# Kernel tuning notes

Measured on AMD Instinct MI355X. Metric: run time of the kernel, lower is better.

The kernel has to match this reference:

```python
import jax, jax.numpy as jnp
import numpy as np

C = 256
HEADS = 8
HD = C // HEADS
EPS = 1e-5


def _layernorm(x, g, b):
    mu = jnp.mean(x, axis=-1, keepdims=True)
    var = jnp.var(x, axis=-1, keepdims=True)
    return (x - mu) * jax.lax.rsqrt(var + EPS) * g + b


def setup_inputs() -> dict:
    key = jax.random.key(0)
    ks = jax.random.split(key, 16)
    s = 0.02
    return {
        "x": jax.random.normal(ks[0], (1, C, 64, 64), jnp.float32),
        "bn_gamma": 1.0 + s * jax.random.normal(ks[1], (C,), jnp.float32),
        "bn_beta": s * jax.random.normal(ks[2], (C,), jnp.float32),
        "bn_mean": s * jax.random.normal(ks[3], (C,), jnp.float32),
        "bn_var": jnp.ones((C,), jnp.float32),
        "w_in": s * jax.random.normal(ks[4], (C, C), jnp.float32),
        "b_in": jnp.zeros((C,), jnp.float32),
        "ln1_g": jnp.ones((C,), jnp.float32),
        "ln1_b": jnp.zeros((C,), jnp.float32),
        "w_qkv": s * jax.random.normal(ks[5], (3 * C, C), jnp.float32),
        "b_qkv": jnp.zeros((3 * C,), jnp.float32),
        "w_ap": s * jax.random.normal(ks[6], (C, C), jnp.float32),
        "b_ap": jnp.zeros((C,), jnp.float32),
        "ln2_g": jnp.ones((C,), jnp.float32),
        "ln2_b": jnp.zeros((C,), jnp.float32),
        "w_ff1": s * jax.random.normal(ks[7], (4 * C, C), jnp.float32),
        "b_ff1": jnp.zeros((4 * C,), jnp.float32),
        "w_ff2": s * jax.random.normal(ks[8], (C, 4 * C), jnp.float32),
        "b_ff2": jnp.zeros((C,), jnp.float32),
        "w_out": s * jax.random.normal(ks[9], (C, C), jnp.float32),
        "b_out": jnp.zeros((C,), jnp.float32),
    }


def reference(x, bn_gamma, bn_beta, bn_mean, bn_var, w_in, b_in,
              ln1_g, ln1_b, w_qkv, b_qkv, w_ap, b_ap,
              ln2_g, ln2_b, w_ff1, b_ff1, w_ff2, b_ff2, w_out, b_out):
    b, c, h, w = x.shape
    t = h * w
    x_in = x
    # BatchNorm2d (eval mode: running stats)
    xn = (x - bn_mean[None, :, None, None]) * jax.lax.rsqrt(bn_var + EPS)[None, :, None, None]
    xn = xn * bn_gamma[None, :, None, None] + bn_beta[None, :, None, None]
    # proj_in 1x1 conv -> tokens [b, t, c]
    tok = xn.reshape(b, c, t).transpose(0, 2, 1)
    tok = tok @ w_in.T + b_in
    # transformer block (depth=1)
    y = _layernorm(tok, ln1_g, ln1_b)  # norm1
    qkv = y @ w_qkv.T + b_qkv  # [b, t, 3c], channel split (3, H, hd)
    qkv = qkv.reshape(b, t, 3, HEADS, HD)
    q = qkv[:, :, 0].transpose(0, 2, 1, 3)  # [b, H, t, hd]
    k = qkv[:, :, 1].transpose(0, 2, 1, 3)
    v = qkv[:, :, 2].transpose(0, 2, 1, 3)
    scale = HD ** (-0.5)
    attn = jax.nn.softmax(jnp.einsum('bhqd,bhkd->bhqk', q, k) * scale, axis=-1)
    o = jnp.einsum('bhqk,bhkd->bhqd', attn, v)  # [b, H, t, hd]
    o = o.transpose(0, 2, 1, 3).reshape(b, t, c)  # channels ordered (H, hd)
    o = o @ w_ap.T + b_ap  # attn proj 1x1
    attn_out = o + y  # VanillaAttention residual adds its (normed) input
    tok = tok + attn_out
    # FFN
    z = _layernorm(tok, ln2_g, ln2_b)
    z = jax.nn.gelu(z @ w_ff1.T + b_ff1, approximate=False)
    tok = tok + (z @ w_ff2.T + b_ff2)
    # back to image, proj_out 1x1, outer residual
    x4 = tok.transpose(0, 2, 1).reshape(b, c, h, w)
    out = jnp.einsum('oc,bchw->bohw', w_out, x4) + b_out[None, :, None, None]
    return out + x_in
```

## Files before the change

kernel.cpp:

```cpp
#include <hip/hip_runtime.h>
#include <math.h>

#define T_TOK 4096
#define C_DIM 256
#define EPSF  1e-5f
#define SC_QL (0.17677669529663687f * 1.4426950408889634f)

typedef short  bf16x8  __attribute__((ext_vector_type(8)));
typedef float  f32x4   __attribute__((ext_vector_type(4)));
typedef ushort ushort8 __attribute__((ext_vector_type(8)));

__device__ __forceinline__ short f2bf(float f) {
    unsigned u = __builtin_bit_cast(unsigned, f);
    unsigned r = (u + 0x7FFFu + ((u >> 16) & 1u)) >> 16;
    return (short)r;
}
__device__ __forceinline__ float bf2f(ushort u) {
    return __builtin_bit_cast(float, ((unsigned)u) << 16);
}
__device__ __forceinline__ unsigned pk_bf16(float a, float b) {
    const unsigned ua = __builtin_bit_cast(unsigned, a) + 0x8000u;
    const unsigned ub = __builtin_bit_cast(unsigned, b) + 0x8000u;
    return __builtin_amdgcn_perm(ub, ua, 0x07060302u);
}
#define MFMA16(a, b, c) __builtin_amdgcn_mfma_f32_16x16x32_bf16(a, b, c, 0, 0, 0)

__global__ __launch_bounds__(256) void prep_kernel(
    const float* __restrict__ w_in, const float* __restrict__ w_qkv,
    const float* __restrict__ w_ap, const float* __restrict__ w_ff1,
    const float* __restrict__ w_ff2, const float* __restrict__ w_out,
    const float* __restrict__ b_qkv, const float* __restrict__ b_ff1,
    const float* __restrict__ ln1_g, const float* __restrict__ ln1_b,
    const float* __restrict__ ln2_g, const float* __restrict__ ln2_b,
    ushort* __restrict__ wbuf, float* __restrict__ u_all, float* __restrict__ d_all,
    const float* __restrict__ x, const float* __restrict__ gamma,
    const float* __restrict__ beta, const float* __restrict__ mean,
    const float* __restrict__ var, ushort* __restrict__ tin)
{
    __shared__ float tile[32][33];
    if (blockIdx.x < 896) {
        const int gid = blockIdx.x * 256 + threadIdx.x;
        const int e0 = gid * 4;
        const float* src; int off;
        float4 sc = {1.f, 1.f, 1.f, 1.f};
        if (e0 < 65536)       { src = w_in;  off = e0; }
        else if (e0 < 262144) {
            src = w_qkv; off = e0 - 65536;
            sc = *(const float4*)(ln1_g + (off & 255));
            if (off < 65536) { sc.x *= SC_QL; sc.y *= SC_QL; sc.z *= SC_QL; sc.w *= SC_QL; }
        }
        else if (e0 < 327680) { src = w_ap;  off = e0 - 262144; }
        else if (e0 < 589824) {
            src = w_ff1; off = e0 - 327680;
            sc = *(const float4*)(ln2_g + (off & 255));
        }
        else if (e0 < 851968) { src = w_ff2; off = e0 - 589824; }
        else                  { src = w_out; off = e0 - 851968; }
        const float4 v = *(const float4*)(src + off);
        ushort4 o;
        o.x = (ushort)f2bf(v.x * sc.x); o.y = (ushort)f2bf(v.y * sc.y);
        o.z = (ushort)f2bf(v.z * sc.z); o.w = (ushort)f2bf(v.w * sc.w);
        *(ushort4*)(wbuf + e0) = o;
    } else if (blockIdx.x < 1920) {
        const int bidx = blockIdx.x - 896;
        const int t0 = (bidx & 127) * 32, c0 = (bidx >> 7) * 32;
        const int tx = threadIdx.x & 31, ty = threadIdx.x >> 5;
#pragma unroll
        for (int i = 0; i < 32; i += 8) {
            const int c = c0 + ty + i;
            const float a = rsqrtf(var[c] + EPSF) * gamma[c];
            const float d = beta[c] - mean[c] * a;
            tile[ty + i][tx] = x[c * T_TOK + t0 + tx] * a + d;
        }
        __syncthreads();
#pragma unroll
        for (int i = 0; i < 32; i += 8) {
            const int t = t0 + ty + i;
            tin[t * C_DIM + c0 + tx] = (ushort)f2bf(tile[tx][ty + i]);
        }
    } else {
        const int row = (blockIdx.x - 1920) * 4 + (threadIdx.x >> 6);
        const int lane = threadIdx.x & 63;
        const float* W; const float* gv; const float* bv; float bias; float qs = 1.f;
        if (row < 768) {
            W = w_qkv + (size_t)row * 256; gv = ln1_g; bv = ln1_b; bias = b_qkv[row];
            if (row < 256) qs = SC_QL;
        } else {
            const int r2 = row - 768;
            W = w_ff1 + (size_t)r2 * 256; gv = ln2_g; bv = ln2_b; bias = b_ff1[r2];
        }
        const float4 w4 = *(const float4*)(W + lane * 4);
        const float4 g4 = *(const float4*)(gv + lane * 4);
        const float4 b4 = *(const float4*)(bv + lane * 4);
        float su = w4.x * g4.x + w4.y * g4.y + w4.z * g4.z + w4.w * g4.w;
        float sd = w4.x * b4.x + w4.y * b4.y + w4.z * b4.z + w4.w * b4.w;
#pragma unroll
        for (int off = 32; off > 0; off >>= 1) {
            su += __shfl_xor(su, off);
            sd += __shfl_xor(sd, off);
        }
        if (lane == 0) {
            u_all[row] = qs * su;
            d_all[row] = qs * (sd + bias);
        }
    }
}

__global__ __launch_bounds__(256) void k_lnstats(
    const float* __restrict__ in, float* __restrict__ st)
{
    const int row = blockIdx.x * 4 + (threadIdx.x >> 6);
    const int lane = threadIdx.x & 63;
    const float4 v = *(const float4*)(in + (size_t)row * 256 + lane * 4);
    float s  = v.x + v.y + v.z + v.w;
    float s2 = v.x * v.x + v.y * v.y + v.z * v.z + v.w * v.w;
#pragma unroll
    for (int off = 32; off > 0; off >>= 1) {
        s  += __shfl_xor(s, off);
        s2 += __shfl_xor(s2, off);
    }
    if (lane == 0) {
        const float mu = s * (1.0f / 256.0f);
        const float var = s2 * (1.0f / 256.0f) - mu * mu;
        st[(size_t)row * 2 + 0] = mu;
        st[(size_t)row * 2 + 1] = rsqrtf(var + EPSF);
    }
}


__global__ __launch_bounds__(256) void k_proj_in(
    const ushort* __restrict__ tin, const ushort* __restrict__ wb,
    const float* __restrict__ bias, float* __restrict__ tok0,
    ushort* __restrict__ vbuf)
{
    __shared__ ushort Wlds[64 * 264];
    __shared__ ushort At[2][16 * 264];
    const int chunk = blockIdx.x & 3, strip = blockIdx.x >> 2;
    const int tid = threadIdx.x, wv = tid >> 6, lane = tid & 63;
    const int c = lane & 15, g = lane >> 4;

    {
        const int wr = tid >> 2, wc = (tid & 3) * 64;
        const ushort* wp = wb + (size_t)(chunk * 64 + wr) * 256 + wc;
#pragma unroll
        for (int i = 0; i < 8; ++i)
            *(ushort8*)&Wlds[wr * 264 + wc + i * 8] = *(const ushort8*)(wp + i * 8);
    }
    const int r = tid >> 4, c0a = (tid & 15) * 16;
    const int t0 = strip * 64;
    ushort8 pre0 = *(const ushort8*)(tin + (size_t)(t0 + r) * 256 + c0a);
    ushort8 pre1 = *(const ushort8*)(tin + (size_t)(t0 + r) * 256 + c0a + 8);

    const int col = chunk * 64 + wv * 16 + c;
    const float bb = bias[col];
    int p = 0;
#pragma unroll
    for (int tile = 0; tile < 4; ++tile) {
        *(ushort8*)&At[p][r * 264 + c0a] = pre0;
        *(ushort8*)&At[p][r * 264 + c0a + 8] = pre1;
        __syncthreads();
        if (tile < 3) {
            pre0 = *(const ushort8*)(tin + (size_t)(t0 + 16 * (tile + 1) + r) * 256 + c0a);
            pre1 = *(const ushort8*)(tin + (size_t)(t0 + 16 * (tile + 1) + r) * 256 + c0a + 8);
        }
        f32x4 acc = {};
#pragma unroll
        for (int kc = 0; kc < 8; ++kc) {
            const bf16x8 af = *(const bf16x8*)&At[p][c * 264 + kc * 32 + g * 8];
            const bf16x8 wf = *(const bf16x8*)&Wlds[(wv * 16 + c) * 264 + kc * 32 + g * 8];
            acc = MFMA16(af, wf, acc);
        }
        const int tt = t0 + tile * 16;
#pragma unroll
        for (int rr = 0; rr < 4; ++rr) {
            const float v = acc[rr] + bb;
            const size_t idx = (size_t)(tt + 4 * g + rr) * 256 + col;
            tok0[idx] = v;
            vbuf[idx] = (ushort)f2bf(v);
        }
        p ^= 1;
    }
}

__global__ __launch_bounds__(256) void k_qkv(
    const ushort* __restrict__ vbuf, const ushort* __restrict__ wb,
    const float* __restrict__ lnst, const float* __restrict__ u_all,
    const float* __restrict__ d_all, ushort* __restrict__ qkvb)
{
    __shared__ ushort Wlds[64 * 264];
    __shared__ ushort At[2][16 * 264];
    const int chunk = blockIdx.x % 12, strip = blockIdx.x / 12;
    const int tid = threadIdx.x, wv = tid >> 6, lane = tid & 63;
    const int c = lane & 15, g = lane >> 4;

    {
        const int wr = tid >> 2, wc = (tid & 3) * 64;
        const ushort* wp = wb + (size_t)(chunk * 64 + wr) * 256 + wc;
#pragma unroll
        for (int i = 0; i < 8; ++i)
            *(ushort8*)&Wlds[wr * 264 + wc + i * 8] = *(const ushort8*)(wp + i * 8);
    }
    const int r = tid >> 4, c0a = (tid & 15) * 16;
    const int t0 = strip * 128;
    ushort8 pre0 = *(const ushort8*)(vbuf + (size_t)(t0 + r) * 256 + c0a);
    ushort8 pre1 = *(const ushort8*)(vbuf + (size_t)(t0 + r) * 256 + c0a + 8);

    const int col = chunk * 64 + wv * 16 + c;
    const float u = u_all[col], d = d_all[col];
    int p = 0;
#pragma unroll 1
    for (int tile = 0; tile < 8; ++tile) {
        *(ushort8*)&At[p][r * 264 + c0a] = pre0;
        *(ushort8*)&At[p][r * 264 + c0a + 8] = pre1;
        __syncthreads();
        if (tile < 7) {
            pre0 = *(const ushort8*)(vbuf + (size_t)(t0 + 16 * (tile + 1) + r) * 256 + c0a);
            pre1 = *(const ushort8*)(vbuf + (size_t)(t0 + 16 * (tile + 1) + r) * 256 + c0a + 8);
        }
        f32x4 acc = {};
#pragma unroll
        for (int kc = 0; kc < 8; ++kc) {
            const bf16x8 af = *(const bf16x8*)&At[p][c * 264 + kc * 32 + g * 8];
            const bf16x8 wf = *(const bf16x8*)&Wlds[(wv * 16 + c) * 264 + kc * 32 + g * 8];
            acc = MFMA16(af, wf, acc);
        }
        const int tt = t0 + tile * 16;
#pragma unroll
        for (int rr = 0; rr < 4; ++rr) {
            const int row = tt + 4 * g + rr;
            const float mu = lnst[(size_t)row * 2 + 0];
            const float rs = lnst[(size_t)row * 2 + 1];
            qkvb[(size_t)row * 768 + col] = (ushort)f2bf(rs * (acc[rr] - mu * u) + d);
        }
        p ^= 1;
    }
}

__global__ __launch_bounds__(256) void k_attnproj(
    const ushort* __restrict__ opart, const float* __restrict__ lpart,
    const ushort* __restrict__ wb, const float* __restrict__ bias,
    const float* __restrict__ tok0, const float* __restrict__ lnst,
    const float* __restrict__ ln1_g, const float* __restrict__ ln1_b,
    float* __restrict__ tok1, ushort* __restrict__ v2buf)
{
    __shared__ ushort Wlds[64 * 264];
    __shared__ ushort At[2][16 * 264];
    const int chunk = blockIdx.x & 3, strip = blockIdx.x >> 2;
    const int tid = threadIdx.x, wv = tid >> 6, lane = tid & 63;
    const int c = lane & 15, g = lane >> 4;

    {
        const int wr = tid >> 2, wc = (tid & 3) * 64;
        const ushort* wp = wb + (size_t)(chunk * 64 + wr) * 256 + wc;
#pragma unroll
        for (int i = 0; i < 8; ++i)
            *(ushort8*)&Wlds[wr * 264 + wc + i * 8] = *(const ushort8*)(wp + i * 8);
    }
    const int r = tid >> 4, c0a = (tid & 15) * 16;
    const int hh = c0a >> 5;
    const int t0 = strip * 64;

    ushort4 pa[4][4];
    float linv;
    {
        const float* lp = lpart + (size_t)(t0 + r) * 32;
        linv = 1.0f / (lp[hh] + lp[8 + hh] + lp[16 + hh] + lp[24 + hh]);
        const size_t base = (size_t)(t0 + r) * 256 + c0a;
#pragma unroll
        for (int cc = 0; cc < 4; ++cc)
#pragma unroll
            for (int q = 0; q < 4; ++q)
                pa[cc][q] = *(const ushort4*)(opart + ((size_t)q << 20) + base + cc * 4);
    }

    const int col = chunk * 64 + wv * 16 + c;
    const float bb = bias[col];
    const float g1 = ln1_g[col], b1 = ln1_b[col];
    int p = 0;
#pragma unroll
    for (int tile = 0; tile < 4; ++tile) {
#pragma unroll
        for (int cc = 0; cc < 4; ++cc) {
            unsigned w[2];
            w[0] = pk_bf16((bf2f(pa[cc][0].x) + bf2f(pa[cc][1].x) + bf2f(pa[cc][2].x) + bf2f(pa[cc][3].x)) * linv,
                           (bf2f(pa[cc][0].y) + bf2f(pa[cc][1].y) + bf2f(pa[cc][2].y) + bf2f(pa[cc][3].y)) * linv);
            w[1] = pk_bf16((bf2f(pa[cc][0].z) + bf2f(pa[cc][1].z) + bf2f(pa[cc][2].z) + bf2f(pa[cc][3].z)) * linv,
                           (bf2f(pa[cc][0].w) + bf2f(pa[cc][1].w) + bf2f(pa[cc][2].w) + bf2f(pa[cc][3].w)) * linv);
            *(ushort4*)&At[p][r * 264 + c0a + cc * 4] = *(ushort4*)w;
        }
        __syncthreads();
        if (tile < 3) {
            const int tn = t0 + 16 * (tile + 1);
            const float* lp = lpart + (size_t)(tn + r) * 32;
            linv = 1.0f / (lp[hh] + lp[8 + hh] + lp[16 + hh] + lp[24 + hh]);
            const size_t base = (size_t)(tn + r) * 256 + c0a;
#pragma unroll
            for (int cc = 0; cc < 4; ++cc)
#pragma unroll
                for (int q = 0; q < 4; ++q)
                    pa[cc][q] = *(const ushort4*)(opart + ((size_t)q << 20) + base + cc * 4);
        }
        f32x4 acc = {};
#pragma unroll
        for (int kc = 0; kc < 8; ++kc) {
            const bf16x8 af = *(const bf16x8*)&At[p][c * 264 + kc * 32 + g * 8];
            const bf16x8 wf = *(const bf16x8*)&Wlds[(wv * 16 + c) * 264 + kc * 32 + g * 8];
            acc = MFMA16(af, wf, acc);
        }
        const int tt = t0 + tile * 16;
#pragma unroll
        for (int rr = 0; rr < 4; ++rr) {
            const int row = tt + 4 * g + rr;
            const size_t idx = (size_t)row * 256 + col;
            const float t0v = tok0[idx];
            const float mu = lnst[(size_t)row * 2 + 0];
            const float rs = lnst[(size_t)row * 2 + 1];
            const float y = (t0v - mu) * rs * g1 + b1;
            const float v = acc[rr] + bb + y + t0v;
            tok1[idx] = v;
            v2buf[idx] = (ushort)f2bf(v);
        }
        p ^= 1;
    }
}

__global__ __launch_bounds__(256) void k_ff1(
    const ushort* __restrict__ v2buf, const ushort* __restrict__ wb,
    const float* __restrict__ lnst, const float* __restrict__ u_all,
    const float* __restrict__ d_all, ushort* __restrict__ zbuf)
{
    __shared__ ushort Wlds[64 * 264];
    __shared__ ushort At[2][16 * 264];
    const int chunk = blockIdx.x & 15, strip = blockIdx.x >> 4;
    const int tid = threadIdx.x, wv = tid >> 6, lane = tid & 63;
    const int c = lane & 15, g = lane >> 4;

    {
        const int wr = tid >> 2, wc = (tid & 3) * 64;
        const ushort* wp = wb + (size_t)(chunk * 64 + wr) * 256 + wc;
#pragma unroll
        for (int i = 0; i < 8; ++i)
            *(ushort8*)&Wlds[wr * 264 + wc + i * 8] = *(const ushort8*)(wp + i * 8);
    }
    const int r = tid >> 4, c0a = (tid & 15) * 16;
    const int t0 = strip * 128;
    ushort8 pre0 = *(const ushort8*)(v2buf + (size_t)(t0 + r) * 256 + c0a);
    ushort8 pre1 = *(const ushort8*)(v2buf + (size_t)(t0 + r) * 256 + c0a + 8);

    const int col = chunk * 64 + wv * 16 + c;
    const float u = u_all[768 + col], d = d_all[768 + col];
    int p = 0;
#pragma unroll 1
    for (int tile = 0; tile < 8; ++tile) {
        *(ushort8*)&At[p][r * 264 + c0a] = pre0;
        *(ushort8*)&At[p][r * 264 + c0a + 8] = pre1;
        __syncthreads();
        if (tile < 7) {
            pre0 = *(const ushort8*)(v2buf + (size_t)(t0 + 16 * (tile + 1) + r) * 256 + c0a);
            pre1 = *(const ushort8*)(v2buf + (size_t)(t0 + 16 * (tile + 1) + r) * 256 + c0a + 8);
        }
        f32x4 acc = {};
#pragma unroll
        for (int kc = 0; kc < 8; ++kc) {
            const bf16x8 af = *(const bf16x8*)&At[p][c * 264 + kc * 32 + g * 8];
            const bf16x8 wf = *(const bf16x8*)&Wlds[(wv * 16 + c) * 264 + kc * 32 + g * 8];
            acc = MFMA16(af, wf, acc);
        }
        const int tt = t0 + tile * 16;
#pragma unroll
        for (int rr = 0; rr < 4; ++rr) {
            const int row = tt + 4 * g + rr;
            const float mu = lnst[(size_t)row * 2 + 0];
            const float rs = lnst[(size_t)row * 2 + 1];
            float v = rs * (acc[rr] - mu * u) + d;
            v = 0.5f * v * (1.0f + erff(v * 0.70710678118654752f));
            zbuf[(size_t)row * 1024 + col] = (ushort)f2bf(v);
        }
        p ^= 1;
    }
}

__global__ __launch_bounds__(256) void k_ff2(
    const ushort* __restrict__ zbuf, const ushort* __restrict__ wb,
    const float* __restrict__ bias, const float* __restrict__ tok1,
    ushort* __restrict__ tok2)
{
    __shared__ ushort Wlds[32 * 1032];
    __shared__ ushort At[32 * 1032];
    const int chunk = blockIdx.x & 7, strip = blockIdx.x >> 3;
    const int tid = threadIdx.x, wv = tid >> 6, lane = tid & 63;
    const int c = lane & 15, g = lane >> 4;

    {
        const int wr = tid >> 3, wc = (tid & 7) * 128;
        const ushort* wp = wb + (size_t)(chunk * 32 + wr) * 1024 + wc;
#pragma unroll
        for (int i = 0; i < 16; ++i)
            *(ushort8*)&Wlds[wr * 1032 + wc + i * 8] = *(const ushort8*)(wp + i * 8);
    }
    const int r = tid >> 3, c0a = (tid & 7) * 128;
    const int t0 = strip * 128;
    ushort8 preZ[16];
#pragma unroll
    for (int i = 0; i < 16; ++i)
        preZ[i] = *(const ushort8*)(zbuf + (size_t)(t0 + r) * 1024 + c0a + i * 8);

    const int sub = wv >> 1, cw = (wv & 1) * 16;
    const int col = chunk * 32 + cw + c;
    const float bb = bias[col];
#pragma unroll 1
    for (int it = 0; it < 4; ++it) {
#pragma unroll
        for (int i = 0; i < 16; ++i)
            *(ushort8*)&At[r * 1032 + c0a + i * 8] = preZ[i];
        __syncthreads();
        if (it < 3) {
            const int tn = t0 + 32 * (it + 1);
#pragma unroll
            for (int i = 0; i < 16; ++i)
                preZ[i] = *(const ushort8*)(zbuf + (size_t)(tn + r) * 1024 + c0a + i * 8);
        }
        f32x4 acc = {};
#pragma unroll
        for (int kc = 0; kc < 32; ++kc) {
            const bf16x8 af = *(const bf16x8*)&At[(sub * 16 + c) * 1032 + kc * 32 + g * 8];
            const bf16x8 wf = *(const bf16x8*)&Wlds[(cw + c) * 1032 + kc * 32 + g * 8];
            acc = MFMA16(af, wf, acc);
        }
        const int tt = t0 + it * 32 + sub * 16;
#pragma unroll
        for (int rr = 0; rr < 4; ++rr) {
            const size_t idx = (size_t)(tt + 4 * g + rr) * 256 + col;
            tok2[idx] = (ushort)f2bf(acc[rr] + bb + tok1[idx]);
        }
        __syncthreads();
    }
}

__global__ __launch_bounds__(256) void k_pout(
    const ushort* __restrict__ tok2, const ushort* __restrict__ wb,
    const float* __restrict__ b_out, const float* __restrict__ x,
    float* __restrict__ out)
{
    __shared__ ushort Wlds[64 * 264];
    __shared__ ushort At[2][16 * 264];
    const int chunk = blockIdx.x & 3, strip = blockIdx.x >> 2;
    const int tid = threadIdx.x, wv = tid >> 6, lane = tid & 63;
    const int c = lane & 15, g = lane >> 4;

    {
        const int wr = tid >> 2, wc = (tid & 3) * 64;
        const ushort* wp = wb + (size_t)(chunk * 64 + wr) * 256 + wc;
#pragma unroll
        for (int i = 0; i < 8; ++i)
            *(ushort8*)&Wlds[wr * 264 + wc + i * 8] = *(const ushort8*)(wp + i * 8);
    }
    const int r = tid >> 4, c0a = (tid & 15) * 16;
    const int t0 = strip * 64;
    ushort8 pre0 = *(const ushort8*)(tok2 + (size_t)(t0 + r) * 256 + c0a);
    ushort8 pre1 = *(const ushort8*)(tok2 + (size_t)(t0 + r) * 256 + c0a + 8);

    int p = 0;
#pragma unroll
    for (int tile = 0; tile < 4; ++tile) {
        *(ushort8*)&At[p][r * 264 + c0a] = pre0;
        *(ushort8*)&At[p][r * 264 + c0a + 8] = pre1;
        __syncthreads();
        if (tile < 3) {
            pre0 = *(const ushort8*)(tok2 + (size_t)(t0 + 16 * (tile + 1) + r) * 256 + c0a);
            pre1 = *(const ushort8*)(tok2 + (size_t)(t0 + 16 * (tile + 1) + r) * 256 + c0a + 8);
        }
        f32x4 acc = {};
#pragma unroll
        for (int kc = 0; kc < 8; ++kc) {
            const bf16x8 wf = *(const bf16x8*)&Wlds[(wv * 16 + c) * 264 + kc * 32 + g * 8];
            const bf16x8 bf = *(const bf16x8*)&At[p][c * 264 + kc * 32 + g * 8];
            acc = MFMA16(wf, bf, acc);
        }
        const int tt = t0 + tile * 16;
#pragma unroll
        for (int rr = 0; rr < 4; ++rr) {
            const int och = chunk * 64 + wv * 16 + 4 * g + rr;
            const size_t idx = (size_t)och * T_TOK + tt + c;
            out[idx] = acc[rr] + b_out[och] + x[idx];
        }
        p ^= 1;
    }
}

#define KS   40
#define VTS  72
#define PS_W 34

__global__ __launch_bounds__(256) void attn_mfma(
    const ushort* __restrict__ qkv, ushort* __restrict__ opart,
    float* __restrict__ lpart)
{
    const int h    = blockIdx.y;
    const int q0   = blockIdx.x << 6;
    const int half = blockIdx.z;
    const int tid  = threadIdx.x;
    const int wv   = tid >> 6, lane = tid & 63;
    const int c    = lane & 15, g = lane >> 4;

    __shared__ ushort Ks[2][64 * KS];
    __shared__ ushort Vt[2][32 * VTS];
    __shared__ float  Ps[4][16 * PS_W];

    const bf16x8 qf = *(const bf16x8*)(qkv + (size_t)(q0 + wv * 16 + c) * 768 + h * 32 + g * 8);

    bf16x8 ones;
#pragma unroll
    for (int i = 0; i < 8; ++i) ones[i] = (short)0x3F80;

    f32x4 oacc0 = {0.f, 0.f, 0.f, 0.f};
    f32x4 oacc1 = {0.f, 0.f, 0.f, 0.f};
    f32x4 oaccl = {0.f, 0.f, 0.f, 0.f};

    const int kr = tid >> 2, kc = (tid & 3) * 8;
    const int vp = tid & 31, vd = (tid >> 5) * 4;
    const ushort* kbase = qkv + 256 + h * 32;
    const ushort* vbase = qkv + 512 + h * 32;

    const int kt0 = half * 16, kt1 = kt0 + 16;
    ushort8 kpre  = *(const ushort8*)(kbase + ((size_t)kt0 * 64 + kr) * 768 + kc);
    ushort4 vpre0 = *(const ushort4*)(vbase + ((size_t)kt0 * 64 + 2 * vp) * 768 + vd);
    ushort4 vpre1 = *(const ushort4*)(vbase + ((size_t)kt0 * 64 + 2 * vp + 1) * 768 + vd);

    int p = 0;
    for (int kt = kt0; kt < kt1; ++kt) {
        *(ushort8*)&Ks[p][kr * KS + kc] = kpre;
        {
            unsigned* vtp = (unsigned*)&Vt[p][0];
            vtp[(vd + 0) * (VTS / 2) + vp] = (unsigned)vpre0.x | ((unsigned)vpre1.x << 16);
            vtp[(vd + 1) * (VTS / 2) + vp] = (unsigned)vpre0.y | ((unsigned)vpre1.y << 16);
            vtp[(vd + 2) * (VTS / 2) + vp] = (unsigned)vpre0.z | ((unsigned)vpre1.z << 16);
            vtp[(vd + 3) * (VTS / 2) + vp] = (unsigned)vpre0.w | ((unsigned)vpre1.w << 16);
        }
        __syncthreads();
        if (kt + 1 < kt1) {
            const size_t t0 = (size_t)(kt + 1) * 64;
            kpre  = *(const ushort8*)(kbase + (t0 + kr) * 768 + kc);
            vpre0 = *(const ushort4*)(vbase + (t0 + 2 * vp) * 768 + vd);
            vpre1 = *(const ushort4*)(vbase + (t0 + 2 * vp + 1) * 768 + vd);
        }

        const ushort* ks = &Ks[p][0];
        const ushort* vt = &Vt[p][0];
        const f32x4 zz = {0.f, 0.f, 0.f, 0.f};
        const bf16x8 k0 = *(const bf16x8*)&ks[(0 * 16 + c) * KS + g * 8];
        const bf16x8 k1 = *(const bf16x8*)&ks[(1 * 16 + c) * KS + g * 8];
        const bf16x8 k2 = *(const bf16x8*)&ks[(2 * 16 + c) * KS + g * 8];
        const bf16x8 k3 = *(const bf16x8*)&ks[(3 * 16 + c) * KS + g * 8];
        const f32x4 s0 = MFMA16(k0, qf, zz);
        const f32x4 s1 = MFMA16(k1, qf, zz);
        const f32x4 s2 = MFMA16(k2, qf, zz);
        const f32x4 s3 = MFMA16(k3, qf, zz);

        float* prow = &Ps[wv][c * PS_W];
        {
            const float e00 = __builtin_amdgcn_exp2f(s0[0]), e01 = __builtin_amdgcn_exp2f(s0[1]);
            const float e02 = __builtin_amdgcn_exp2f(s0[2]), e03 = __builtin_amdgcn_exp2f(s0[3]);
            const float e10 = __builtin_amdgcn_exp2f(s1[0]), e11 = __builtin_amdgcn_exp2f(s1[1]);
            const float e12 = __builtin_amdgcn_exp2f(s1[2]), e13 = __builtin_amdgcn_exp2f(s1[3]);
            const float e20 = __builtin_amdgcn_exp2f(s2[0]), e21 = __builtin_amdgcn_exp2f(s2[1]);
            const float e22 = __builtin_amdgcn_exp2f(s2[2]), e23 = __builtin_amdgcn_exp2f(s2[3]);
            const float e30 = __builtin_amdgcn_exp2f(s3[0]), e31 = __builtin_amdgcn_exp2f(s3[1]);
            const float e32 = __builtin_amdgcn_exp2f(s3[2]), e33 = __builtin_amdgcn_exp2f(s3[3]);
            prow[0 * 8 + 2 * g + 0] = __builtin_bit_cast(float, pk_bf16(e00, e01));
            prow[0 * 8 + 2 * g + 1] = __builtin_bit_cast(float, pk_bf16(e02, e03));
            prow[1 * 8 + 2 * g + 0] = __builtin_bit_cast(float, pk_bf16(e10, e11));
            prow[1 * 8 + 2 * g + 1] = __builtin_bit_cast(float, pk_bf16(e12, e13));
            prow[2 * 8 + 2 * g + 0] = __builtin_bit_cast(float, pk_bf16(e20, e21));
            prow[2 * 8 + 2 * g + 1] = __builtin_bit_cast(float, pk_bf16(e22, e23));
            prow[3 * 8 + 2 * g + 0] = __builtin_bit_cast(float, pk_bf16(e30, e31));
            prow[3 * 8 + 2 * g + 1] = __builtin_bit_cast(float, pk_bf16(e32, e33));
        }
#pragma unroll
        for (int ch = 0; ch < 2; ++ch) {
            const float2 pA = *(const float2*)&prow[ch * 16 + 4 * g];
            const float2 pB = *(const float2*)&prow[ch * 16 + 4 * g + 2];
            unsigned pw[4];
            pw[0] = __builtin_bit_cast(unsigned, pA.x);
            pw[1] = __builtin_bit_cast(unsigned, pA.y);
            pw[2] = __builtin_bit_cast(unsigned, pB.x);
            pw[3] = __builtin_bit_cast(unsigned, pB.y);
            const bf16x8 pf = *(const bf16x8*)pw;
            const bf16x8 v0 = *(const bf16x8*)&vt[(c)      * VTS + ch * 32 + g * 8];
            const bf16x8 v1 = *(const bf16x8*)&vt[(16 + c) * VTS + ch * 32 + g * 8];
            oacc0 = MFMA16(pf, v0, oacc0);
            oacc1 = MFMA16(pf, v1, oacc1);
            oaccl = MFMA16(pf, ones, oaccl);
        }
        p ^= 1;
        __syncthreads();
    }

    {
        ushort* op = opart + (size_t)half * (1u << 20) + (size_t)(q0 + wv * 16) * 256 + h * 32;
#pragma unroll
        for (int rr = 0; rr < 4; ++rr) {
            op[(4 * g + rr) * 256 + c]      = (ushort)f2bf(oacc0[rr]);
            op[(4 * g + rr) * 256 + 16 + c] = (ushort)f2bf(oacc1[rr]);
        }
        if (c == 0) {
#pragma unroll
            for (int rr = 0; rr < 4; ++rr)
                lpart[(size_t)(q0 + wv * 16 + 4 * g + rr) * 32 + half * 8 + h] = oaccl[rr];
        }
    }
}

extern "C" void kernel_launch(void* const* d_in, const int* in_sizes, int n_in,
                              void* d_out, int out_size, void* d_ws, size_t ws_size,
                              hipStream_t stream)
{
    const float* x     = (const float*)d_in[0];
    const float* bn_g  = (const float*)d_in[1];
    const float* bn_b  = (const float*)d_in[2];
    const float* bn_m  = (const float*)d_in[3];
    const float* bn_v  = (const float*)d_in[4];
    const float* w_in  = (const float*)d_in[5];
    const float* b_in  = (const float*)d_in[6];
    const float* ln1_g = (const float*)d_in[7];
    const float* ln1_b = (const float*)d_in[8];
    const float* w_qkv = (const float*)d_in[9];
    const float* b_qkv = (const float*)d_in[10];
    const float* w_ap  = (const float*)d_in[11];
    const float* b_ap  = (const float*)d_in[12];
    const float* ln2_g = (const float*)d_in[13];
    const float* ln2_b = (const float*)d_in[14];
    const float* w_ff1 = (const float*)d_in[15];
    const float* b_ff1 = (const float*)d_in[16];
    const float* w_ff2 = (const float*)d_in[17];
    const float* b_ff2 = (const float*)d_in[18];
    const float* w_out = (const float*)d_in[19];
    const float* b_out = (const float*)d_in[20];
    float* out = (float*)d_out;
    float* ws  = (float*)d_ws;

    const size_t MF = 1u << 20;
    float*  tok0   = ws;
    float*  tok1   = ws + MF;
    float*  lnst1  = ws + 2 * MF;
    float*  lnst2  = ws + 2 * MF + 8192;
    ushort* tok2   = (ushort*)(ws + 2 * MF + MF / 4);
    ushort* vbuf   = (ushort*)(ws + 2 * MF + MF / 2);
    ushort* qkv_bf = (ushort*)(ws + 3 * MF);
    ushort* tin_bf = (ushort*)(ws + 4 * MF + MF / 2);
    ushort* opart  = tin_bf;
    ushort* v2buf  = (ushort*)(ws + 6 * MF + MF / 2);
    ushort* zbuf   = (ushort*)(ws + 7 * MF);
    float*  lpart  = ws + 9 * MF;
    ushort* wbuf   = (ushort*)(ws + 9 * MF + 131072);
    const ushort* wb_in  = wbuf;
    const ushort* wb_qkv = wbuf + 65536;
    const ushort* wb_ap  = wbuf + 262144;
    const ushort* wb_ff1 = wbuf + 327680;
    const ushort* wb_ff2 = wbuf + 589824;
    const ushort* wb_out = wbuf + 851968;
    float* u_all = (float*)(wbuf + 917504);
    float* d_all = u_all + 1792;

    prep_kernel<<<2368, 256, 0, stream>>>(
        w_in, w_qkv, w_ap, w_ff1, w_ff2, w_out,
        b_qkv, b_ff1, ln1_g, ln1_b, ln2_g, ln2_b,
        wbuf, u_all, d_all,
        x, bn_g, bn_b, bn_m, bn_v, tin_bf);
    k_proj_in<<<256, 256, 0, stream>>>(tin_bf, wb_in, b_in, tok0, vbuf);
    k_lnstats<<<1024, 256, 0, stream>>>(tok0, lnst1);
    k_qkv<<<384, 256, 0, stream>>>(vbuf, wb_qkv, lnst1, u_all, d_all, qkv_bf);
    attn_mfma<<<dim3(64, 8, 4), 256, 0, stream>>>(qkv_bf, opart, lpart);
    k_attnproj<<<256, 256, 0, stream>>>(opart, lpart, wb_ap, b_ap, tok0, lnst1,
                                        ln1_g, ln1_b, tok1, v2buf);
    k_lnstats<<<1024, 256, 0, stream>>>(tok1, lnst2);
    k_ff1<<<512, 256, 0, stream>>>(v2buf, wb_ff1, lnst2, u_all, d_all, zbuf);
    k_ff2<<<256, 256, 0, stream>>>(zbuf, wb_ff2, b_ff2, tok1, tok2);
    k_pout<<<256, 256, 0, stream>>>(tok2, wb_out, b_out, x, out);
}
```

Measured before the change: 215.1 us.

## Hold weights in registers, shrink token strips, split-K FF2 with fused residual in pout

```diff
diff --git a/kernel.cpp b/kernel.cpp
--- a/kernel.cpp
+++ b/kernel.cpp
@@ -133,52 +133,34 @@
     const float* __restrict__ bias, float* __restrict__ tok0,
     ushort* __restrict__ vbuf)
 {
-    __shared__ ushort Wlds[64 * 264];
-    __shared__ ushort At[2][16 * 264];
+    __shared__ ushort At[16 * 264];
     const int chunk = blockIdx.x & 3, strip = blockIdx.x >> 2;
     const int tid = threadIdx.x, wv = tid >> 6, lane = tid & 63;
     const int c = lane & 15, g = lane >> 4;
-
+    const int col = chunk * 64 + wv * 16 + c;
+    const int t0 = strip * 16;
+
+    bf16x8 w[8];
+#pragma unroll
+    for (int kc = 0; kc < 8; ++kc)
+        w[kc] = *(const bf16x8*)(wb + (size_t)col * 256 + kc * 32 + g * 8);
     {
-        const int wr = tid >> 2, wc = (tid & 3) * 64;
-        const ushort* wp = wb + (size_t)(chunk * 64 + wr) * 256 + wc;
-#pragma unroll
-        for (int i = 0; i < 8; ++i)
-            *(ushort8*)&Wlds[wr * 264 + wc + i * 8] = *(const ushort8*)(wp + i * 8);
-    }
-    const int r = tid >> 4, c0a = (tid & 15) * 16;
-    const int t0 = strip * 64;
-    ushort8 pre0 = *(const ushort8*)(tin + (size_t)(t0 + r) * 256 + c0a);
-    ushort8 pre1 = *(const ushort8*)(tin + (size_t)(t0 + r) * 256 + c0a + 8);
-
-    const int col = chunk * 64 + wv * 16 + c;
+        const int r = tid >> 4, c0 = (tid & 15) * 16;
+        *(ushort8*)&At[r * 264 + c0]     = *(const ushort8*)(tin + (size_t)(t0 + r) * 256 + c0);
+        *(ushort8*)&At[r * 264 + c0 + 8] = *(const ushort8*)(tin + (size_t)(t0 + r) * 256 + c0 + 8);
+    }
+    __syncthreads();
+    f32x4 acc = {};
+#pragma unroll
+    for (int kc = 0; kc < 8; ++kc)
+        acc = MFMA16(*(const bf16x8*)&At[c * 264 + kc * 32 + g * 8], w[kc], acc);
     const float bb = bias[col];
-    int p = 0;
-#pragma unroll
-    for (int tile = 0; tile < 4; ++tile) {
-        *(ushort8*)&At[p][r * 264 + c0a] = pre0;
-        *(ushort8*)&At[p][r * 264 + c0a + 8] = pre1;
-        __syncthreads();
-        if (tile < 3) {
-            pre0 = *(const ushort8*)(tin + (size_t)(t0 + 16 * (tile + 1) + r) * 256 + c0a);
-            pre1 = *(const ushort8*)(tin + (size_t)(t0 + 16 * (tile + 1) + r) * 256 + c0a + 8);
-        }
-        f32x4 acc = {};
-#pragma unroll
-        for (int kc = 0; kc < 8; ++kc) {
-            const bf16x8 af = *(const bf16x8*)&At[p][c * 264 + kc * 32 + g * 8];
-            const bf16x8 wf = *(const bf16x8*)&Wlds[(wv * 16 + c) * 264 + kc * 32 + g * 8];
-            acc = MFMA16(af, wf, acc);
-        }
-        const int tt = t0 + tile * 16;
-#pragma unroll
-        for (int rr = 0; rr < 4; ++rr) {
-            const float v = acc[rr] + bb;
-            const size_t idx = (size_t)(tt + 4 * g + rr) * 256 + col;
-            tok0[idx] = v;
-            vbuf[idx] = (ushort)f2bf(v);
-        }
-        p ^= 1;
+#pragma unroll
+    for (int rr = 0; rr < 4; ++rr) {
+        const float v = acc[rr] + bb;
+        const size_t idx = (size_t)(t0 + 4 * g + rr) * 256 + col;
+        tok0[idx] = v;
+        vbuf[idx] = (ushort)f2bf(v);
     }
 }
 
@@ -187,43 +169,35 @@
     const float* __restrict__ lnst, const float* __restrict__ u_all,
     const float* __restrict__ d_all, ushort* __restrict__ qkvb)
 {
-    __shared__ ushort Wlds[64 * 264];
     __shared__ ushort At[2][16 * 264];
     const int chunk = blockIdx.x % 12, strip = blockIdx.x / 12;
     const int tid = threadIdx.x, wv = tid >> 6, lane = tid & 63;
     const int c = lane & 15, g = lane >> 4;
-
-    {
-        const int wr = tid >> 2, wc = (tid & 3) * 64;
-        const ushort* wp = wb + (size_t)(chunk * 64 + wr) * 256 + wc;
-#pragma unroll
-        for (int i = 0; i < 8; ++i)
-            *(ushort8*)&Wlds[wr * 264 + wc + i * 8] = *(const ushort8*)(wp + i * 8);
-    }
-    const int r = tid >> 4, c0a = (tid & 15) * 16;
-    const int t0 = strip * 128;
-    ushort8 pre0 = *(const ushort8*)(vbuf + (size_t)(t0 + r) * 256 + c0a);
-    ushort8 pre1 = *(const ushort8*)(vbuf + (size_t)(t0 + r) * 256 + c0a + 8);
-
     const int col = chunk * 64 + wv * 16 + c;
+    const int t0 = strip * 32;
+    const int r = tid >> 4, c0 = (tid & 15) * 16;
+
+    bf16x8 w[8];
+#pragma unroll
+    for (int kc = 0; kc < 8; ++kc)
+        w[kc] = *(const bf16x8*)(wb + (size_t)col * 256 + kc * 32 + g * 8);
+    ushort8 pre0 = *(const ushort8*)(vbuf + (size_t)(t0 + r) * 256 + c0);
+    ushort8 pre1 = *(const ushort8*)(vbuf + (size_t)(t0 + r) * 256 + c0 + 8);
+
     const float u = u_all[col], d = d_all[col];
-    int p = 0;
-#pragma unroll 1
-    for (int tile = 0; tile < 8; ++tile) {
-        *(ushort8*)&At[p][r * 264 + c0a] = pre0;
-        *(ushort8*)&At[p][r * 264 + c0a + 8] = pre1;
+#pragma unroll
+    for (int tile = 0; tile < 2; ++tile) {
+        *(ushort8*)&At[tile][r * 264 + c0]     = pre0;
+        *(ushort8*)&At[tile][r * 264 + c0 + 8] = pre1;
         __syncthreads();
-        if (tile < 7) {
-            pre0 = *(const ushort8*)(vbuf + (size_t)(t0 + 16 * (tile + 1) + r) * 256 + c0a);
-            pre1 = *(const ushort8*)(vbuf + (size_t)(t0 + 16 * (tile + 1) + r) * 256 + c0a + 8);
+        if (tile == 0) {
+            pre0 = *(const ushort8*)(vbuf + (size_t)(t0 + 16 + r) * 256 + c0);
+            pre1 = *(const ushort8*)(vbuf + (size_t)(t0 + 16 + r) * 256 + c0 + 8);
         }
         f32x4 acc = {};
 #pragma unroll
-        for (int kc = 0; kc < 8; ++kc) {
-            const bf16x8 af = *(const bf16x8*)&At[p][c * 264 + kc * 32 + g * 8];
-            const bf16x8 wf = *(const bf16x8*)&Wlds[(wv * 16 + c) * 264 + kc * 32 + g * 8];
-            acc = MFMA16(af, wf, acc);
-        }
+        for (int kc = 0; kc < 8; ++kc)
+            acc = MFMA16(*(const bf16x8*)&At[tile][c * 264 + kc * 32 + g * 8], w[kc], acc);
         const int tt = t0 + tile * 16;
 #pragma unroll
         for (int rr = 0; rr < 4; ++rr) {
@@ -232,7 +206,6 @@
             const float rs = lnst[(size_t)row * 2 + 1];
             qkvb[(size_t)row * 768 + col] = (ushort)f2bf(rs * (acc[rr] - mu * u) + d);
         }
-        p ^= 1;
     }
 }
 
@@ -243,84 +216,55 @@
     const float* __restrict__ ln1_g, const float* __restrict__ ln1_b,
     float* __restrict__ tok1, ushort* __restrict__ v2buf)
 {
-    __shared__ ushort Wlds[64 * 264];
-    __shared__ ushort At[2][16 * 264];
+    __shared__ ushort At[16 * 264];
     const int chunk = blockIdx.x & 3, strip = blockIdx.x >> 2;
     const int tid = threadIdx.x, wv = tid >> 6, lane = tid & 63;
     const int c = lane & 15, g = lane >> 4;
-
+    const int col = chunk * 64 + wv * 16 + c;
+    const int t0 = strip * 16;
+
+    bf16x8 w[8];
+#pragma unroll
+    for (int kc = 0; kc < 8; ++kc)
+        w[kc] = *(const bf16x8*)(wb + (size_t)col * 256 + kc * 32 + g * 8);
     {
-        const int wr = tid >> 2, wc = (tid & 3) * 64;
-        const ushort* wp = wb + (size_t)(chunk * 64 + wr) * 256 + wc;
-#pragma unroll
-        for (int i = 0; i < 8; ++i)
-            *(ushort8*)&Wlds[wr * 264 + wc + i * 8] = *(const ushort8*)(wp + i * 8);
-    }
-    const int r = tid >> 4, c0a = (tid & 15) * 16;
-    const int hh = c0a >> 5;
-    const int t0 = strip * 64;
-
-    ushort4 pa[4][4];
-    float linv;
-    {
+        const int r = tid >> 4, c0 = (tid & 15) * 16;
+        const int hh = c0 >> 5;
         const float* lp = lpart + (size_t)(t0 + r) * 32;
-        linv = 1.0f / (lp[hh] + lp[8 + hh] + lp[16 + hh] + lp[24 + hh]);
-        const size_t base = (size_t)(t0 + r) * 256 + c0a;
-#pragma unroll
-        for (int cc = 0; cc < 4; ++cc)
-#pragma unroll
-            for (int q = 0; q < 4; ++q)
-                pa[cc][q] = *(const ushort4*)(opart + ((size_t)q << 20) + base + cc * 4);
-    }
-
-    const int col = chunk * 64 + wv * 16 + c;
+        const float inv = 1.0f / (lp[hh] + lp[8 + hh] + lp[16 + hh] + lp[24 + hh]);
+        const size_t base = (size_t)(t0 + r) * 256 + c0;
+#pragma unroll
+        for (int cc = 0; cc < 4; ++cc) {
+            const ushort4 a0 = *(const ushort4*)(opart + base + cc * 4);
+            const ushort4 a1 = *(const ushort4*)(opart + (1u << 20) + base + cc * 4);
+            const ushort4 a2 = *(const ushort4*)(opart + (2u << 20) + base + cc * 4);
+            const ushort4 a3 = *(const ushort4*)(opart + (3u << 20) + base + cc * 4);
+            unsigned wpk[2];
+            wpk[0] = pk_bf16((bf2f(a0.x) + bf2f(a1.x) + bf2f(a2.x) + bf2f(a3.x)) * inv,
+                             (bf2f(a0.y) + bf2f(a1.y) + bf2f(a2.y) + bf2f(a3.y)) * inv);
+            wpk[1] = pk_bf16((bf2f(a0.z) + bf2f(a1.z) + bf2f(a2.z) + bf2f(a3.z)) * inv,
+                             (bf2f(a0.w) + bf2f(a1.w) + bf2f(a2.w) + bf2f(a3.w)) * inv);
+            *(ushort4*)&At[r * 264 + c0 + cc * 4] = *(ushort4*)wpk;
+        }
+    }
+    __syncthreads();
+    f32x4 acc = {};
+#pragma unroll
+    for (int kc = 0; kc < 8; ++kc)
+        acc = MFMA16(*(const bf16x8*)&At[c * 264 + kc * 32 + g * 8], w[kc], acc);
     const float bb = bias[col];
     const float g1 = ln1_g[col], b1 = ln1_b[col];
-    int p = 0;
-#pragma unroll
-    for (int tile = 0; tile < 4; ++tile) {
-#pragma unroll
-        for (int cc = 0; cc < 4; ++cc) {
-            unsigned w[2];
-            w[0] = pk_bf16((bf2f(pa[cc][0].x) + bf2f(pa[cc][1].x) + bf2f(pa[cc][2].x) + bf2f(pa[cc][3].x)) * linv,
-                           (bf2f(pa[cc][0].y) + bf2f(pa[cc][1].y) + bf2f(pa[cc][2].y) + bf2f(pa[cc][3].y)) * linv);
-            w[1] = pk_bf16((bf2f(pa[cc][0].z) + bf2f(pa[cc][1].z) + bf2f(pa[cc][2].z) + bf2f(pa[cc][3].z)) * linv,
-                           (bf2f(pa[cc][0].w) + bf2f(pa[cc][1].w) + bf2f(pa[cc][2].w) + bf2f(pa[cc][3].w)) * linv);
-            *(ushort4*)&At[p][r * 264 + c0a + cc * 4] = *(ushort4*)w;
-        }
-        __syncthreads();
-        if (tile < 3) {
-            const int tn = t0 + 16 * (tile + 1);
-            const float* lp = lpart + (size_t)(tn + r) * 32;
-            linv = 1.0f / (lp[hh] + lp[8 + hh] + lp[16 + hh] + lp[24 + hh]);
-            const size_t base = (size_t)(tn + r) * 256 + c0a;
-#pragma unroll
-            for (int cc = 0; cc < 4; ++cc)
-#pragma unroll
-                for (int q = 0; q < 4; ++q)
-                    pa[cc][q] = *(const ushort4*)(opart + ((size_t)q << 20) + base + cc * 4);
-        }
-        f32x4 acc = {};
-#pragma unroll
-        for (int kc = 0; kc < 8; ++kc) {
-            const bf16x8 af = *(const bf16x8*)&At[p][c * 264 + kc * 32 + g * 8];
-            const bf16x8 wf = *(const bf16x8*)&Wlds[(wv * 16 + c) * 264 + kc * 32 + g * 8];
-            acc = MFMA16(af, wf, acc);
-        }
-        const int tt = t0 + tile * 16;
-#pragma unroll
-        for (int rr = 0; rr < 4; ++rr) {
-            const int row = tt + 4 * g + rr;
-            const size_t idx = (size_t)row * 256 + col;
-            const float t0v = tok0[idx];
-            const float mu = lnst[(size_t)row * 2 + 0];
-            const float rs = lnst[(size_t)row * 2 + 1];
-            const float y = (t0v - mu) * rs * g1 + b1;
-            const float v = acc[rr] + bb + y + t0v;
-            tok1[idx] = v;
-            v2buf[idx] = (ushort)f2bf(v);
-        }
-        p ^= 1;
+#pragma unroll
+    for (int rr = 0; rr < 4; ++rr) {
+        const int row = t0 + 4 * g + rr;
+        const size_t idx = (size_t)row * 256 + col;
+        const float t0v = tok0[idx];
+        const float mu = lnst[(size_t)row * 2 + 0];
+        const float rs = lnst[(size_t)row * 2 + 1];
+        const float y = (t0v - mu) * rs * g1 + b1;
+        const float v = acc[rr] + bb + y + t0v;
+        tok1[idx] = v;
+        v2buf[idx] = (ushort)f2bf(v);
     }
 }
 
@@ -329,43 +273,35 @@
     const float* __restrict__ lnst, const float* __restrict__ u_all,
     const float* __restrict__ d_all, ushort* __restrict__ zbuf)
 {
-    __shared__ ushort Wlds[64 * 264];
     __shared__ ushort At[2][16 * 264];
     const int chunk = blockIdx.x & 15, strip = blockIdx.x >> 4;
     const int tid = threadIdx.x, wv = tid >> 6, lane = tid & 63;
     const int c = lane & 15, g = lane >> 4;
-
-    {
-        const int wr = tid >> 2, wc = (tid & 3) * 64;
-        const ushort* wp = wb + (size_t)(chunk * 64 + wr) * 256 + wc;
-#pragma unroll
-        for (int i = 0; i < 8; ++i)
-            *(ushort8*)&Wlds[wr * 264 + wc + i * 8] = *(const ushort8*)(wp + i * 8);
-    }
-    const int r = tid >> 4, c0a = (tid & 15) * 16;
-    const int t0 = strip * 128;
-    ushort8 pre0 = *(const ushort8*)(v2buf + (size_t)(t0 + r) * 256 + c0a);
-    ushort8 pre1 = *(const ushort8*)(v2buf + (size_t)(t0 + r) * 256 + c0a + 8);
-
     const int col = chunk * 64 + wv * 16 + c;
+    const int t0 = strip * 32;
+    const int r = tid >> 4, c0 = (tid & 15) * 16;
+
+    bf16x8 w[8];
+#pragma unroll
+    for (int kc = 0; kc < 8; ++kc)
+        w[kc] = *(const bf16x8*)(wb + (size_t)col * 256 + kc * 32 + g * 8);
+    ushort8 pre0 = *(const ushort8*)(v2buf + (size_t)(t0 + r) * 256 + c0);
+    ushort8 pre1 = *(const ushort8*)(v2buf + (size_t)(t0 + r) * 256 + c0 + 8);
+
     const float u = u_all[768 + col], d = d_all[768 + col];
-    int p = 0;
-#pragma unroll 1
-    for (int tile = 0; tile < 8; ++tile) {
-        *(ushort8*)&At[p][r * 264 + c0a] = pre0;
-        *(ushort8*)&At[p][r * 264 + c0a + 8] = pre1;
+#pragma unroll
+    for (int tile = 0; tile < 2; ++tile) {
+        *(ushort8*)&At[tile][r * 264 + c0]     = pre0;
+        *(ushort8*)&At[tile][r * 264 + c0 + 8] = pre1;
         __syncthreads();
-        if (tile < 7) {
-            pre0 = *(const ushort8*)(v2buf + (size_t)(t0 + 16 * (tile + 1) + r) * 256 + c0a);
-            pre1 = *(const ushort8*)(v2buf + (size_t)(t0 + 16 * (tile + 1) + r) * 256 + c0a + 8);
+        if (tile == 0) {
+            pre0 = *(const ushort8*)(v2buf + (size_t)(t0 + 16 + r) * 256 + c0);
+            pre1 = *(const ushort8*)(v2buf + (size_t)(t0 + 16 + r) * 256 + c0 + 8);
         }
         f32x4 acc = {};
 #pragma unroll
-        for (int kc = 0; kc < 8; ++kc) {
-            const bf16x8 af = *(const bf16x8*)&At[p][c * 264 + kc * 32 + g * 8];
-            const bf16x8 wf = *(const bf16x8*)&Wlds[(wv * 16 + c) * 264 + kc * 32 + g * 8];
-            acc = MFMA16(af, wf, acc);
-        }
+        for (int kc = 0; kc < 8; ++kc)
+            acc = MFMA16(*(const bf16x8*)&At[tile][c * 264 + kc * 32 + g * 8], w[kc], acc);
         const int tt = t0 + tile * 16;
 #pragma unroll
         for (int rr = 0; rr < 4; ++rr) {
@@ -376,115 +312,96 @@
             v = 0.5f * v * (1.0f + erff(v * 0.70710678118654752f));
             zbuf[(size_t)row * 1024 + col] = (ushort)f2bf(v);
         }
-        p ^= 1;
     }
 }
 
 __global__ __launch_bounds__(256) void k_ff2(
     const ushort* __restrict__ zbuf, const ushort* __restrict__ wb,
-    const float* __restrict__ bias, const float* __restrict__ tok1,
-    ushort* __restrict__ tok2)
-{
-    __shared__ ushort Wlds[32 * 1032];
-    __shared__ ushort At[32 * 1032];
-    const int chunk = blockIdx.x & 7, strip = blockIdx.x >> 3;
+    float* __restrict__ pf2)
+{
+    __shared__ ushort At[2][16 * 520];
+    const int chunk = blockIdx.x & 3, half = (blockIdx.x >> 2) & 1, strip = blockIdx.x >> 3;
     const int tid = threadIdx.x, wv = tid >> 6, lane = tid & 63;
     const int c = lane & 15, g = lane >> 4;
-
-    {
-        const int wr = tid >> 3, wc = (tid & 7) * 128;
-        const ushort* wp = wb + (size_t)(chunk * 32 + wr) * 1024 + wc;
-#pragma unroll
-        for (int i = 0; i < 16; ++i)
-            *(ushort8*)&Wlds[wr * 1032 + wc + i * 8] = *(const ushort8*)(wp + i * 8);
-    }
-    const int r = tid >> 3, c0a = (tid & 7) * 128;
-    const int t0 = strip * 128;
-    ushort8 preZ[16];
-#pragma unroll
-    for (int i = 0; i < 16; ++i)
-        preZ[i] = *(const ushort8*)(zbuf + (size_t)(t0 + r) * 1024 + c0a + i * 8);
-
-    const int sub = wv >> 1, cw = (wv & 1) * 16;
-    const int col = chunk * 32 + cw + c;
-    const float bb = bias[col];
-#pragma unroll 1
-    for (int it = 0; it < 4; ++it) {
-#pragma unroll
-        for (int i = 0; i < 16; ++i)
-            *(ushort8*)&At[r * 1032 + c0a + i * 8] = preZ[i];
+    const int col = chunk * 64 + wv * 16 + c;
+    const int t0 = strip * 32;
+    const int r = tid >> 4, c0 = (tid & 15) * 32;
+
+    bf16x8 w[16];
+#pragma unroll
+    for (int kc = 0; kc < 16; ++kc)
+        w[kc] = *(const bf16x8*)(wb + (size_t)col * 1024 + half * 512 + kc * 32 + g * 8);
+    const ushort* zsrc = zbuf + half * 512;
+    ushort8 pre[4];
+#pragma unroll
+    for (int i = 0; i < 4; ++i)
+        pre[i] = *(const ushort8*)(zsrc + (size_t)(t0 + r) * 1024 + c0 + i * 8);
+
+#pragma unroll
+    for (int tile = 0; tile < 2; ++tile) {
+#pragma unroll
+        for (int i = 0; i < 4; ++i)
+            *(ushort8*)&At[tile][r * 520 + c0 + i * 8] = pre[i];
         __syncthreads();
-        if (it < 3) {
-            const int tn = t0 + 32 * (it + 1);
-#pragma unroll
-            for (int i = 0; i < 16; ++i)
-                preZ[i] = *(const ushort8*)(zbuf + (size_t)(tn + r) * 1024 + c0a + i * 8);
+        if (tile == 0) {
+#pragma unroll
+            for (int i = 0; i < 4; ++i)
+                pre[i] = *(const ushort8*)(zsrc + (size_t)(t0 + 16 + r) * 1024 + c0 + i * 8);
         }
         f32x4 acc = {};
 #pragma unroll
-        for (int kc = 0; kc < 32; ++kc) {
-            const bf16x8 af = *(const bf16x8*)&At[(sub * 16 + c) * 1032 + kc * 32 + g * 8];
-            const bf16x8 wf = *(const bf16x8*)&Wlds[(cw + c) * 1032 + kc * 32 + g * 8];
-            acc = MFMA16(af, wf, acc);
-        }
-        const int tt = t0 + it * 32 + sub * 16;
-#pragma unroll
-        for (int rr = 0; rr < 4; ++rr) {
-            const size_t idx = (size_t)(tt + 4 * g + rr) * 256 + col;
-            tok2[idx] = (ushort)f2bf(acc[rr] + bb + tok1[idx]);
-        }
-        __syncthreads();
+        for (int kc = 0; kc < 16; ++kc)
+            acc = MFMA16(*(const bf16x8*)&At[tile][c * 520 + kc * 32 + g * 8], w[kc], acc);
+        const int tt = t0 + tile * 16;
+        float* op = pf2 + (size_t)half * (1u << 20);
+#pragma unroll
+        for (int rr = 0; rr < 4; ++rr)
+            op[(size_t)(tt + 4 * g + rr) * 256 + col] = acc[rr];
     }
 }
 
 __global__ __launch_bounds__(256) void k_pout(
-    const ushort* __restrict__ tok2, const ushort* __restrict__ wb,
+    const float* __restrict__ pf2, const float* __restrict__ b_ff2,
+    const float* __restrict__ tok1, const ushort* __restrict__ wb,
     const float* __restrict__ b_out, const float* __restrict__ x,
     float* __restrict__ out)
 {
-    __shared__ ushort Wlds[64 * 264];
-    __shared__ ushort At[2][16 * 264];
+    __shared__ ushort At[16 * 264];
     const int chunk = blockIdx.x & 3, strip = blockIdx.x >> 2;
     const int tid = threadIdx.x, wv = tid >> 6, lane = tid & 63;
     const int c = lane & 15, g = lane >> 4;
-
+    const int t0 = strip * 16;
+
+    bf16x8 w[8];
+#pragma unroll
+    for (int kc = 0; kc < 8; ++kc)
+        w[kc] = *(const bf16x8*)(wb +
+            (size_t)(chunk * 64 + wv * 16 + c) * 256 + kc * 32 + g * 8);
     {
-        const int wr = tid >> 2, wc = (tid & 3) * 64;
-        const ushort* wp = wb + (size_t)(chunk * 64 + wr) * 256 + wc;
-#pragma unroll
-        for (int i = 0; i < 8; ++i)
-            *(ushort8*)&Wlds[wr * 264 + wc + i * 8] = *(const ushort8*)(wp + i * 8);
-    }
-    const int r = tid >> 4, c0a = (tid & 15) * 16;
-    const int t0 = strip * 64;
-    ushort8 pre0 = *(const ushort8*)(tok2 + (size_t)(t0 + r) * 256 + c0a);
-    ushort8 pre1 = *(const ushort8*)(tok2 + (size_t)(t0 + r) * 256 + c0a + 8);
-
-    int p = 0;
-#pragma unroll
-    for (int tile = 0; tile < 4; ++tile) {
-        *(ushort8*)&At[p][r * 264 + c0a] = pre0;
-        *(ushort8*)&At[p][r * 264 + c0a + 8] = pre1;
-        __syncthreads();
-        if (tile < 3) {
-            pre0 = *(const ushort8*)(tok2 + (size_t)(t0 + 16 * (tile + 1) + r) * 256 + c0a);
-            pre1 = *(const ushort8*)(tok2 + (size_t)(t0 + 16 * (tile + 1) + r) * 256 + c0a + 8);
-        }
-        f32x4 acc = {};
-#pragma unroll
-        for (int kc = 0; kc < 8; ++kc) {
-            const bf16x8 wf = *(const bf16x8*)&Wlds[(wv * 16 + c) * 264 + kc * 32 + g * 8];
-            const bf16x8 bf = *(const bf16x8*)&At[p][c * 264 + kc * 32 + g * 8];
-            acc = MFMA16(wf, bf, acc);
-        }
-        const int tt = t0 + tile * 16;
-#pragma unroll
-        for (int rr = 0; rr < 4; ++rr) {
-            const int och = chunk * 64 + wv * 16 + 4 * g + rr;
-            const size_t idx = (size_t)och * T_TOK + tt + c;
-            out[idx] = acc[rr] + b_out[och] + x[idx];
-        }
-        p ^= 1;
+        const int r = tid >> 4, c0 = (tid & 15) * 16;
+        const size_t base = (size_t)(t0 + r) * 256 + c0;
+#pragma unroll
+        for (int q = 0; q < 4; ++q) {
+            const float4 p0 = *(const float4*)(pf2 + base + q * 4);
+            const float4 p1 = *(const float4*)(pf2 + (1u << 20) + base + q * 4);
+            const float4 tk = *(const float4*)(tok1 + base + q * 4);
+            const float4 bf = *(const float4*)(b_ff2 + c0 + q * 4);
+            unsigned wpk[2];
+            wpk[0] = pk_bf16(p0.x + p1.x + bf.x + tk.x, p0.y + p1.y + bf.y + tk.y);
+            wpk[1] = pk_bf16(p0.z + p1.z + bf.z + tk.z, p0.w + p1.w + bf.w + tk.w);
+            *(ushort4*)&At[r * 264 + c0 + q * 4] = *(ushort4*)wpk;
+        }
+    }
+    __syncthreads();
+    f32x4 acc = {};
+#pragma unroll
+    for (int kc = 0; kc < 8; ++kc)
+        acc = MFMA16(w[kc], *(const bf16x8*)&At[c * 264 + kc * 32 + g * 8], acc);
+#pragma unroll
+    for (int rr = 0; rr < 4; ++rr) {
+        const int och = chunk * 64 + wv * 16 + 4 * g + rr;
+        const size_t idx = (size_t)och * T_TOK + t0 + c;
+        out[idx] = acc[rr] + b_out[och] + x[idx];
     }
 }
 
@@ -644,7 +561,6 @@
     float*  tok1   = ws + MF;
     float*  lnst1  = ws + 2 * MF;
     float*  lnst2  = ws + 2 * MF + 8192;
-    ushort* tok2   = (ushort*)(ws + 2 * MF + MF / 4);
     ushort* vbuf   = (ushort*)(ws + 2 * MF + MF / 2);
     ushort* qkv_bf = (ushort*)(ws + 3 * MF);
     ushort* tin_bf = (ushort*)(ws + 4 * MF + MF / 2);
@@ -652,7 +568,8 @@
     ushort* v2buf  = (ushort*)(ws + 6 * MF + MF / 2);
     ushort* zbuf   = (ushort*)(ws + 7 * MF);
     float*  lpart  = ws + 9 * MF;
-    ushort* wbuf   = (ushort*)(ws + 9 * MF + 131072);
+    float*  pf2    = ws + 9 * MF + MF / 4;
+    ushort* wbuf   = (ushort*)(ws + 11 * MF + MF / 2);
     const ushort* wb_in  = wbuf;
     const ushort* wb_qkv = wbuf + 65536;
     const ushort* wb_ap  = wbuf + 262144;
@@ -667,14 +584,14 @@
         b_qkv, b_ff1, ln1_g, ln1_b, ln2_g, ln2_b,
         wbuf, u_all, d_all,
         x, bn_g, bn_b, bn_m, bn_v, tin_bf);
-    k_proj_in<<<256, 256, 0, stream>>>(tin_bf, wb_in, b_in, tok0, vbuf);
+    k_proj_in<<<1024, 256, 0, stream>>>(tin_bf, wb_in, b_in, tok0, vbuf);
     k_lnstats<<<1024, 256, 0, stream>>>(tok0, lnst1);
-    k_qkv<<<384, 256, 0, stream>>>(vbuf, wb_qkv, lnst1, u_all, d_all, qkv_bf);
+    k_qkv<<<1536, 256, 0, stream>>>(vbuf, wb_qkv, lnst1, u_all, d_all, qkv_bf);
     attn_mfma<<<dim3(64, 8, 4), 256, 0, stream>>>(qkv_bf, opart, lpart);
-    k_attnproj<<<256, 256, 0, stream>>>(opart, lpart, wb_ap, b_ap, tok0, lnst1,
-                                        ln1_g, ln1_b, tok1, v2buf);
+    k_attnproj<<<1024, 256, 0, stream>>>(opart, lpart, wb_ap, b_ap, tok0, lnst1,
+                                         ln1_g, ln1_b, tok1, v2buf);
     k_lnstats<<<1024, 256, 0, stream>>>(tok1, lnst2);
-    k_ff1<<<512, 256, 0, stream>>>(v2buf, wb_ff1, lnst2, u_all, d_all, zbuf);
-    k_ff2<<<256, 256, 0, stream>>>(zbuf, wb_ff2, b_ff2, tok1, tok2);
-    k_pout<<<256, 256, 0, stream>>>(tok2, wb_out, b_out, x, out);
-}
+    k_ff1<<<2048, 256, 0, stream>>>(v2buf, wb_ff1, lnst2, u_all, d_all, zbuf);
+    k_ff2<<<1024, 256, 0, stream>>>(zbuf, wb_ff2, pf2);
+    k_pout<<<1024, 256, 0, stream>>>(pf2, b_ff2, tok1, wb_out, b_out, x, out);
+}
```

Result: faster. 210.6 us (-2.1%).
